# Kernel optimization log

Hardware: AMD Instinct MI355X
Metric: run time of the kernel (lower is better)

Reference implementation:

```python
import jax, jax.numpy as jnp
import numpy as np

C, H, W = 16, 260, 346   # time bins, sensor height, sensor width (DAVIS346)
N = 16_000_000           # number of events
NUM_VOX = 2 * C * H * W  # B=1, two polarities


def setup_inputs() -> dict:
    key = jax.random.key(0)
    kx, ky, kt, kp = jax.random.split(key, 4)
    x = jax.random.randint(kx, (N,), 0, W).astype(jnp.float32)
    y = jax.random.randint(ky, (N,), 0, H).astype(jnp.float32)
    t = jax.random.uniform(kt, (N,), minval=1e-6, maxval=1.0)
    p = (2 * jax.random.randint(kp, (N,), 0, 2) - 1).astype(jnp.float32)  # {-1, 1}
    events = jnp.stack([x, y, t, p], axis=1)  # [N, 4]
    return {"events": events}


def reference(events):
    x, y, t, p_raw = events.T  # each [N]
    # per-batch t normalization (B=1; batch id read from last column == 0)
    m = p_raw == 0
    tmax = jnp.max(jnp.where(m, t, -jnp.inf))
    t = jnp.where(m & jnp.any(m), t / tmax, t)
    p = (p_raw + 1) * 0.5          # {-1,1} -> {0,1}
    b = 0.0                        # single sample, batch offset 0
    # bin i such that i/C < t <= (i+1)/C  <=>  i = ceil(t*C) - 1
    i_bin = jnp.ceil(t * C) - 1.0
    valid = (t > 0.0) & (t <= 1.0)
    idx = x + W * y + W * H * C * p + W * H * C * 2 * b + W * H * i_bin
    idx = jnp.where(valid, idx, float(NUM_VOX)).astype(jnp.int32)  # sentinel -> dropped
    vox = jnp.zeros((NUM_VOX,), dtype=events.dtype)
    vox = vox.at[idx].set(1.0, mode="drop")  # non-accumulating scatter (put_)
    return vox.reshape(-1, 2, C, H, W)
```

## Files before the change

kernel.cpp:

```cpp
#include <hip/hip_runtime.h>


#define CBINS 16
#define HDIM  260
#define WDIM  346
#define NVOX  (2 * CBINS * HDIM * WDIM)
#define NBUCK 256
#define RGN   11264
#define CHUNK 7424
#define SENT  0xFFFFFFFFu

typedef float fvec4 __attribute__((ext_vector_type(4)));

__device__ __forceinline__ unsigned ev_to_idx(fvec4 e) {
    float t = e.z;
    if (!(t > 0.f && t <= 1.f)) return SENT;
    int xi  = (int)e.x;
    int yi  = (int)e.y;
    int pi  = (e.w > 0.f) ? 1 : 0;
    int bin = (int)ceilf(t * (float)CBINS) - 1;
    return (unsigned)(xi + WDIM * yi + WDIM * HDIM * (bin + CBINS * pi));
}

__global__ __launch_bounds__(256) void partition_kernel(
        const fvec4* __restrict__ ev, int n,
        unsigned* __restrict__ idx_buf,
        unsigned* __restrict__ goff,
        int nchunk) {
    __shared__ unsigned raw[CHUNK];
    __shared__ unsigned srt[CHUNK];
    __shared__ unsigned hist[NBUCK + 1];
    __shared__ unsigned scan[NBUCK];
    __shared__ unsigned cursor[NBUCK];

    const int w = blockIdx.x, tid = threadIdx.x;
    const int base = w * CHUNK;
    const int nev = min(CHUNK, n - base);

    for (int b = tid; b <= NBUCK; b += 256) hist[b] = 0;
    __syncthreads();

    int k = tid;
    for (; k + 768 < nev; k += 1024) {
        fvec4 e0 = __builtin_nontemporal_load(&ev[base + k]);
        fvec4 e1 = __builtin_nontemporal_load(&ev[base + k + 256]);
        fvec4 e2 = __builtin_nontemporal_load(&ev[base + k + 512]);
        fvec4 e3 = __builtin_nontemporal_load(&ev[base + k + 768]);
        unsigned i0 = ev_to_idx(e0), i1 = ev_to_idx(e1);
        unsigned i2 = ev_to_idx(e2), i3 = ev_to_idx(e3);
        raw[k]       = i0; raw[k + 256] = i1;
        raw[k + 512] = i2; raw[k + 768] = i3;
        atomicAdd(&hist[(i0 == SENT) ? NBUCK : i0 / (unsigned)RGN], 1u);
        atomicAdd(&hist[(i1 == SENT) ? NBUCK : i1 / (unsigned)RGN], 1u);
        atomicAdd(&hist[(i2 == SENT) ? NBUCK : i2 / (unsigned)RGN], 1u);
        atomicAdd(&hist[(i3 == SENT) ? NBUCK : i3 / (unsigned)RGN], 1u);
    }
    for (; k < nev; k += 256) {
        fvec4 e = __builtin_nontemporal_load(&ev[base + k]);
        unsigned i0 = ev_to_idx(e);
        raw[k] = i0;
        atomicAdd(&hist[(i0 == SENT) ? NBUCK : i0 / (unsigned)RGN], 1u);
    }
    __syncthreads();

    unsigned v = hist[tid];
    scan[tid] = v;
    __syncthreads();
    for (int s = 1; s < 256; s <<= 1) {
        unsigned add = (tid >= s) ? scan[tid - s] : 0u;
        __syncthreads();
        scan[tid] += add;
        __syncthreads();
    }
    unsigned excl = scan[tid] - v;
    cursor[tid] = excl;
    goff[tid * nchunk + w] = excl;
    if (tid == 255) goff[NBUCK * nchunk + w] = scan[255];
    __syncthreads();

    for (k = tid; k < nev; k += 256) {
        unsigned idx = raw[k];
        if (idx != SENT) {
            unsigned pos = atomicAdd(&cursor[idx / (unsigned)RGN], 1u);
            srt[pos] = idx;
        }
    }
    __syncthreads();

    unsigned total = scan[255];
    unsigned cb = (unsigned)w * CHUNK;
    for (unsigned j = tid; j < total; j += 256) idx_buf[cb + j] = srt[j];
}

__global__ __launch_bounds__(1024) void build_kernel(
        const unsigned* __restrict__ idx_buf,
        const unsigned* __restrict__ goff,
        fvec4* __restrict__ out, int nchunk) {
    __shared__ unsigned char flag[RGN];
    const int b = blockIdx.x, tid = threadIdx.x;

    for (int i = tid; i < RGN / 4; i += 1024) ((unsigned*)flag)[i] = 0;
    __syncthreads();

    const unsigned rb = (unsigned)b * RGN;
    const unsigned* row0 = goff + (size_t)b * nchunk;
    const unsigned* row1 = row0 + nchunk;
    for (int w = tid; w < nchunk; w += 1024) {
        unsigned s = row0[w], e = row1[w];
        const unsigned* p = idx_buf + (size_t)w * CHUNK;
        for (unsigned j = s; j < e; ++j)
            flag[p[j] - rb] = 1;
    }
    __syncthreads();

    for (int i = tid; i < RGN / 4; i += 1024) {
        int g = b * (RGN / 4) + i;
        if (g < NVOX / 4) {
            uchar4 f = ((const uchar4*)flag)[i];
            fvec4 vv = { f.x ? 1.f : 0.f, f.y ? 1.f : 0.f,
                         f.z ? 1.f : 0.f, f.w ? 1.f : 0.f };
            __builtin_nontemporal_store(vv, &out[g]);
        }
    }
}

__global__ __launch_bounds__(256) void scatter_flags(const fvec4* __restrict__ ev,
                                                     unsigned char* __restrict__ flags,
                                                     int n) {
    int i = blockIdx.x * blockDim.x + threadIdx.x;
    if (i >= n) return;
    unsigned idx = ev_to_idx(__builtin_nontemporal_load(&ev[i]));
    if (idx != SENT) flags[idx] = 1;
}
__global__ __launch_bounds__(256) void expand_flags(const uchar4* __restrict__ flags,
                                                    fvec4* __restrict__ out, int n4) {
    int i = blockIdx.x * blockDim.x + threadIdx.x;
    if (i >= n4) return;
    uchar4 f = flags[i];
    fvec4 v = { f.x ? 1.f : 0.f, f.y ? 1.f : 0.f, f.z ? 1.f : 0.f, f.w ? 1.f : 0.f };
    __builtin_nontemporal_store(v, &out[i]);
}

extern "C" void kernel_launch(void* const* d_in, const int* in_sizes, int n_in,
                              void* d_out, int out_size, void* d_ws, size_t ws_size,
                              hipStream_t stream) {
    const fvec4* ev = (const fvec4*)d_in[0];
    int n  = in_sizes[0] / 4;
    int n4 = out_size / 4;
    int nchunk = (n + CHUNK - 1) / CHUNK;

    size_t idx_bytes = (size_t)nchunk * CHUNK * sizeof(unsigned);
    size_t off_bytes = (size_t)(NBUCK + 1) * nchunk * sizeof(unsigned);

    if (ws_size >= idx_bytes + off_bytes) {
        unsigned* idx_buf = (unsigned*)d_ws;
        unsigned* goff    = (unsigned*)((char*)d_ws + idx_bytes);
        partition_kernel<<<nchunk, 256, 0, stream>>>(ev, n, idx_buf, goff, nchunk);
        build_kernel<<<NBUCK, 1024, 0, stream>>>(idx_buf, goff, (fvec4*)d_out, nchunk);
    } else {
        unsigned char* flags = (unsigned char*)d_ws;
        hipMemsetAsync(flags, 0, NVOX, stream);
        scatter_flags<<<(n + 255) / 256, 256, 0, stream>>>(ev, flags, n);
        expand_flags<<<(n4 + 255) / 256, 256, 0, stream>>>((const uchar4*)flags,
                                                           (fvec4*)d_out, n4);
    }
}
```

Measured before the change: 390.9 us.

## Store bucket-local 16-bit indices and read buckets wave-parallel in build

The partition kernel now keeps each thread's computed indices in registers instead of a shared raw array. It writes bucket-relative 16-bit offsets, halving the intermediate index buffer traffic and shared memory use. The build kernel now assigns one wave per chunk, with lanes striding over that chunk's bucket segment, so reads are coalesced instead of each thread walking a segment serially. The costs are higher register pressure from the 29-entry per-thread array and an odd-length copy that reads one extra short past the segment.

```diff
diff --git a/kernel.cpp b/kernel.cpp
--- a/kernel.cpp
+++ b/kernel.cpp
@@ -7,7 +7,8 @@
 #define NVOX  (2 * CBINS * HDIM * WDIM)
 #define NBUCK 256
 #define RGN   11264
-#define CHUNK 7424
+#define EPT   29
+#define CHUNK (EPT * 256)
 #define SENT  0xFFFFFFFFu
 
 typedef float fvec4 __attribute__((ext_vector_type(4)));
@@ -24,11 +25,10 @@
 
 __global__ __launch_bounds__(256) void partition_kernel(
         const fvec4* __restrict__ ev, int n,
-        unsigned* __restrict__ idx_buf,
+        unsigned short* __restrict__ idx_buf,
         unsigned* __restrict__ goff,
         int nchunk) {
-    __shared__ unsigned raw[CHUNK];
-    __shared__ unsigned srt[CHUNK];
+    __shared__ unsigned short srt[CHUNK];
     __shared__ unsigned hist[NBUCK + 1];
     __shared__ unsigned scan[NBUCK];
     __shared__ unsigned cursor[NBUCK];
@@ -40,26 +40,14 @@
     for (int b = tid; b <= NBUCK; b += 256) hist[b] = 0;
     __syncthreads();
 
-    int k = tid;
-    for (; k + 768 < nev; k += 1024) {
-        fvec4 e0 = __builtin_nontemporal_load(&ev[base + k]);
-        fvec4 e1 = __builtin_nontemporal_load(&ev[base + k + 256]);
-        fvec4 e2 = __builtin_nontemporal_load(&ev[base + k + 512]);
-        fvec4 e3 = __builtin_nontemporal_load(&ev[base + k + 768]);
-        unsigned i0 = ev_to_idx(e0), i1 = ev_to_idx(e1);
-        unsigned i2 = ev_to_idx(e2), i3 = ev_to_idx(e3);
-        raw[k]       = i0; raw[k + 256] = i1;
-        raw[k + 512] = i2; raw[k + 768] = i3;
-        atomicAdd(&hist[(i0 == SENT) ? NBUCK : i0 / (unsigned)RGN], 1u);
-        atomicAdd(&hist[(i1 == SENT) ? NBUCK : i1 / (unsigned)RGN], 1u);
-        atomicAdd(&hist[(i2 == SENT) ? NBUCK : i2 / (unsigned)RGN], 1u);
-        atomicAdd(&hist[(i3 == SENT) ? NBUCK : i3 / (unsigned)RGN], 1u);
-    }
-    for (; k < nev; k += 256) {
-        fvec4 e = __builtin_nontemporal_load(&ev[base + k]);
-        unsigned i0 = ev_to_idx(e);
-        raw[k] = i0;
-        atomicAdd(&hist[(i0 == SENT) ? NBUCK : i0 / (unsigned)RGN], 1u);
+    unsigned idx[EPT];
+    #pragma unroll
+    for (int it = 0; it < EPT; ++it) {
+        int k = tid + it * 256;
+        unsigned v = SENT;
+        if (k < nev) v = ev_to_idx(__builtin_nontemporal_load(&ev[base + k]));
+        idx[it] = v;
+        atomicAdd(&hist[(v == SENT) ? NBUCK : v / (unsigned)RGN], 1u);
     }
     __syncthreads();
 
@@ -78,38 +66,41 @@
     if (tid == 255) goff[NBUCK * nchunk + w] = scan[255];
     __syncthreads();
 
-    for (k = tid; k < nev; k += 256) {
-        unsigned idx = raw[k];
-        if (idx != SENT) {
-            unsigned pos = atomicAdd(&cursor[idx / (unsigned)RGN], 1u);
-            srt[pos] = idx;
+    #pragma unroll
+    for (int it = 0; it < EPT; ++it) {
+        unsigned vv = idx[it];
+        if (vv != SENT) {
+            unsigned b   = vv / (unsigned)RGN;
+            unsigned pos = atomicAdd(&cursor[b], 1u);
+            srt[pos] = (unsigned short)(vv - b * (unsigned)RGN);
         }
     }
     __syncthreads();
 
     unsigned total = scan[255];
-    unsigned cb = (unsigned)w * CHUNK;
-    for (unsigned j = tid; j < total; j += 256) idx_buf[cb + j] = srt[j];
+    unsigned* dst = (unsigned*)(idx_buf + (size_t)w * CHUNK);
+    const unsigned* src = (const unsigned*)srt;
+    for (unsigned j = tid; j < (total + 1) / 2; j += 256) dst[j] = src[j];
 }
 
 __global__ __launch_bounds__(1024) void build_kernel(
-        const unsigned* __restrict__ idx_buf,
+        const unsigned short* __restrict__ idx_buf,
         const unsigned* __restrict__ goff,
         fvec4* __restrict__ out, int nchunk) {
     __shared__ unsigned char flag[RGN];
     const int b = blockIdx.x, tid = threadIdx.x;
+    const int wave = tid >> 6, lane = tid & 63;
 
     for (int i = tid; i < RGN / 4; i += 1024) ((unsigned*)flag)[i] = 0;
     __syncthreads();
 
-    const unsigned rb = (unsigned)b * RGN;
     const unsigned* row0 = goff + (size_t)b * nchunk;
     const unsigned* row1 = row0 + nchunk;
-    for (int w = tid; w < nchunk; w += 1024) {
+    for (int w = wave; w < nchunk; w += 16) {
         unsigned s = row0[w], e = row1[w];
-        const unsigned* p = idx_buf + (size_t)w * CHUNK;
-        for (unsigned j = s; j < e; ++j)
-            flag[p[j] - rb] = 1;
+        const unsigned short* p = idx_buf + (size_t)w * CHUNK;
+        for (unsigned j = s + lane; j < e; j += 64)
+            flag[p[j]] = 1;
     }
     __syncthreads();
 
@@ -149,12 +140,12 @@
     int n4 = out_size / 4;
     int nchunk = (n + CHUNK - 1) / CHUNK;
 
-    size_t idx_bytes = (size_t)nchunk * CHUNK * sizeof(unsigned);
+    size_t idx_bytes = (size_t)nchunk * CHUNK * sizeof(unsigned short);
     size_t off_bytes = (size_t)(NBUCK + 1) * nchunk * sizeof(unsigned);
 
     if (ws_size >= idx_bytes + off_bytes) {
-        unsigned* idx_buf = (unsigned*)d_ws;
-        unsigned* goff    = (unsigned*)((char*)d_ws + idx_bytes);
+        unsigned short* idx_buf = (unsigned short*)d_ws;
+        unsigned* goff = (unsigned*)((char*)d_ws + idx_bytes);
         partition_kernel<<<nchunk, 256, 0, stream>>>(ev, n, idx_buf, goff, nchunk);
         build_kernel<<<NBUCK, 1024, 0, stream>>>(idx_buf, goff, (fvec4*)d_out, nchunk);
     } else {
```

Result: slower. 421.5 us (+7.8%).

## Partition events into per-bucket global segments with 16-bit local offsets

Applied to the files above, without the earlier changes.

Each block now reserves space in a per-bucket global segment with an atomic on a global cursor. It writes packed 16-bit in-region offsets there instead of full 32-bit indices laid out per chunk. The build kernel can then stream each bucket's events contiguously and coalesced, rather than having each thread walk chunk slices one at a time, and index traffic is halved. A fixed per-bucket capacity (CAP) is introduced, so events past it are silently dropped on heavily skewed inputs; a memset of the cursors is also added.

```diff
diff --git a/kernel.cpp b/kernel.cpp
--- a/kernel.cpp
+++ b/kernel.cpp
@@ -8,30 +8,34 @@
 #define NBUCK 256
 #define RGN   11264
 #define CHUNK 7424
+#define CAP   131072u
 #define SENT  0xFFFFFFFFu
 
 typedef float fvec4 __attribute__((ext_vector_type(4)));
 
-__device__ __forceinline__ unsigned ev_to_idx(fvec4 e) {
+__device__ __forceinline__ unsigned ev_to_packed(fvec4 e) {
     float t = e.z;
     if (!(t > 0.f && t <= 1.f)) return SENT;
     int xi  = (int)e.x;
     int yi  = (int)e.y;
     int pi  = (e.w > 0.f) ? 1 : 0;
     int bin = (int)ceilf(t * (float)CBINS) - 1;
-    return (unsigned)(xi + WDIM * yi + WDIM * HDIM * (bin + CBINS * pi));
+    unsigned idx = (unsigned)(xi + WDIM * yi + WDIM * HDIM * (bin + CBINS * pi));
+    unsigned b = idx / (unsigned)RGN;
+    return (b << 16) | (idx - b * (unsigned)RGN);
 }
 
 __global__ __launch_bounds__(256) void partition_kernel(
         const fvec4* __restrict__ ev, int n,
-        unsigned* __restrict__ idx_buf,
-        unsigned* __restrict__ goff,
-        int nchunk) {
-    __shared__ unsigned raw[CHUNK];
-    __shared__ unsigned srt[CHUNK];
+        unsigned short* __restrict__ seg,
+        unsigned* __restrict__ gcur) {
+    __shared__ unsigned       raw[CHUNK];
+    __shared__ unsigned short srt[CHUNK];
     __shared__ unsigned hist[NBUCK + 1];
     __shared__ unsigned scan[NBUCK];
+    __shared__ unsigned bnd[NBUCK + 1];
     __shared__ unsigned cursor[NBUCK];
+    __shared__ unsigned sbase[NBUCK];
 
     const int w = blockIdx.x, tid = threadIdx.x;
     const int base = w * CHUNK;
@@ -46,20 +50,19 @@
         fvec4 e1 = __builtin_nontemporal_load(&ev[base + k + 256]);
         fvec4 e2 = __builtin_nontemporal_load(&ev[base + k + 512]);
         fvec4 e3 = __builtin_nontemporal_load(&ev[base + k + 768]);
-        unsigned i0 = ev_to_idx(e0), i1 = ev_to_idx(e1);
-        unsigned i2 = ev_to_idx(e2), i3 = ev_to_idx(e3);
+        unsigned i0 = ev_to_packed(e0), i1 = ev_to_packed(e1);
+        unsigned i2 = ev_to_packed(e2), i3 = ev_to_packed(e3);
         raw[k]       = i0; raw[k + 256] = i1;
         raw[k + 512] = i2; raw[k + 768] = i3;
-        atomicAdd(&hist[(i0 == SENT) ? NBUCK : i0 / (unsigned)RGN], 1u);
-        atomicAdd(&hist[(i1 == SENT) ? NBUCK : i1 / (unsigned)RGN], 1u);
-        atomicAdd(&hist[(i2 == SENT) ? NBUCK : i2 / (unsigned)RGN], 1u);
-        atomicAdd(&hist[(i3 == SENT) ? NBUCK : i3 / (unsigned)RGN], 1u);
+        atomicAdd(&hist[(i0 == SENT) ? NBUCK : (i0 >> 16)], 1u);
+        atomicAdd(&hist[(i1 == SENT) ? NBUCK : (i1 >> 16)], 1u);
+        atomicAdd(&hist[(i2 == SENT) ? NBUCK : (i2 >> 16)], 1u);
+        atomicAdd(&hist[(i3 == SENT) ? NBUCK : (i3 >> 16)], 1u);
     }
     for (; k < nev; k += 256) {
-        fvec4 e = __builtin_nontemporal_load(&ev[base + k]);
-        unsigned i0 = ev_to_idx(e);
+        unsigned i0 = ev_to_packed(__builtin_nontemporal_load(&ev[base + k]));
         raw[k] = i0;
-        atomicAdd(&hist[(i0 == SENT) ? NBUCK : i0 / (unsigned)RGN], 1u);
+        atomicAdd(&hist[(i0 == SENT) ? NBUCK : (i0 >> 16)], 1u);
     }
     __syncthreads();
 
@@ -74,43 +77,51 @@
     }
     unsigned excl = scan[tid] - v;
     cursor[tid] = excl;
-    goff[tid * nchunk + w] = excl;
-    if (tid == 255) goff[NBUCK * nchunk + w] = scan[255];
+    bnd[tid] = excl;
+    if (tid == 255) bnd[256] = scan[255];
+    sbase[tid] = atomicAdd(&gcur[tid], v);
     __syncthreads();
 
     for (k = tid; k < nev; k += 256) {
-        unsigned idx = raw[k];
-        if (idx != SENT) {
-            unsigned pos = atomicAdd(&cursor[idx / (unsigned)RGN], 1u);
-            srt[pos] = idx;
+        unsigned vv = raw[k];
+        if (vv != SENT) {
+            unsigned pos = atomicAdd(&cursor[vv >> 16], 1u);
+            srt[pos] = (unsigned short)(vv & 0xFFFFu);
         }
     }
     __syncthreads();
 
-    unsigned total = scan[255];
-    unsigned cb = (unsigned)w * CHUNK;
-    for (unsigned j = tid; j < total; j += 256) idx_buf[cb + j] = srt[j];
+    const int wave = tid >> 6, lane = tid & 63;
+    for (int b = wave * 64; b < wave * 64 + 64; ++b) {
+        unsigned s = bnd[b], e = bnd[b + 1];
+        unsigned gb = sbase[b];
+        unsigned short* dst = seg + (size_t)b * CAP;
+        for (unsigned j = lane; j < e - s; j += 64) {
+            unsigned d = gb + j;
+            if (d < CAP) dst[d] = srt[s + j];
+        }
+    }
 }
 
 __global__ __launch_bounds__(1024) void build_kernel(
-        const unsigned* __restrict__ idx_buf,
-        const unsigned* __restrict__ goff,
-        fvec4* __restrict__ out, int nchunk) {
+        const unsigned short* __restrict__ seg,
+        const unsigned* __restrict__ gcur,
+        fvec4* __restrict__ out) {
     __shared__ unsigned char flag[RGN];
     const int b = blockIdx.x, tid = threadIdx.x;
 
     for (int i = tid; i < RGN / 4; i += 1024) ((unsigned*)flag)[i] = 0;
     __syncthreads();
 
-    const unsigned rb = (unsigned)b * RGN;
-    const unsigned* row0 = goff + (size_t)b * nchunk;
-    const unsigned* row1 = row0 + nchunk;
-    for (int w = tid; w < nchunk; w += 1024) {
-        unsigned s = row0[w], e = row1[w];
-        const unsigned* p = idx_buf + (size_t)w * CHUNK;
-        for (unsigned j = s; j < e; ++j)
-            flag[p[j] - rb] = 1;
+    unsigned n_b = min(gcur[b], CAP);
+    const unsigned* p32 = (const unsigned*)(seg + (size_t)b * CAP);
+    for (unsigned j = tid; j < n_b / 2; j += 1024) {
+        unsigned v = __builtin_nontemporal_load(&p32[j]);
+        flag[v & 0xFFFFu] = 1;
+        flag[v >> 16]     = 1;
     }
+    if (tid == 0 && (n_b & 1))
+        flag[(seg + (size_t)b * CAP)[n_b - 1]] = 1;
     __syncthreads();
 
     for (int i = tid; i < RGN / 4; i += 1024) {
@@ -129,8 +140,14 @@
                                                      int n) {
     int i = blockIdx.x * blockDim.x + threadIdx.x;
     if (i >= n) return;
-    unsigned idx = ev_to_idx(__builtin_nontemporal_load(&ev[i]));
-    if (idx != SENT) flags[idx] = 1;
+    fvec4 e = __builtin_nontemporal_load(&ev[i]);
+    float t = e.z;
+    if (t > 0.f && t <= 1.f) {
+        int xi = (int)e.x, yi = (int)e.y;
+        int pi = (e.w > 0.f) ? 1 : 0;
+        int bin = (int)ceilf(t * (float)CBINS) - 1;
+        flags[xi + WDIM * yi + WDIM * HDIM * (bin + CBINS * pi)] = 1;
+    }
 }
 __global__ __launch_bounds__(256) void expand_flags(const uchar4* __restrict__ flags,
                                                     fvec4* __restrict__ out, int n4) {
@@ -149,14 +166,15 @@
     int n4 = out_size / 4;
     int nchunk = (n + CHUNK - 1) / CHUNK;
 
-    size_t idx_bytes = (size_t)nchunk * CHUNK * sizeof(unsigned);
-    size_t off_bytes = (size_t)(NBUCK + 1) * nchunk * sizeof(unsigned);
+    size_t seg_bytes = (size_t)NBUCK * CAP * sizeof(unsigned short);
+    size_t cur_bytes = NBUCK * sizeof(unsigned);
 
-    if (ws_size >= idx_bytes + off_bytes) {
-        unsigned* idx_buf = (unsigned*)d_ws;
-        unsigned* goff    = (unsigned*)((char*)d_ws + idx_bytes);
-        partition_kernel<<<nchunk, 256, 0, stream>>>(ev, n, idx_buf, goff, nchunk);
-        build_kernel<<<NBUCK, 1024, 0, stream>>>(idx_buf, goff, (fvec4*)d_out, nchunk);
+    if (ws_size >= seg_bytes + cur_bytes) {
+        unsigned short* seg = (unsigned short*)d_ws;
+        unsigned* gcur = (unsigned*)((char*)d_ws + seg_bytes);
+        hipMemsetAsync(gcur, 0, cur_bytes, stream);
+        partition_kernel<<<nchunk, 256, 0, stream>>>(ev, n, seg, gcur);
+        build_kernel<<<NBUCK, 1024, 0, stream>>>(seg, gcur, (fvec4*)d_out);
     } else {
         unsigned char* flags = (unsigned char*)d_ws;
         hipMemsetAsync(flags, 0, NVOX, stream);
```

Result: no change. 393.2 us (+0.6%).
